# Kernel tuning notes

Hardware: AMD Instinct MI355X
Metric: run time of the kernel (lower is better)

Reference implementation:

```python
import jax, jax.numpy as jnp
import numpy as np

N, E, DIN, EDIM = 50000, 500000, 64, 32
H, C, L, NG = 4, 64, 2, 64
ND = 64  # node_dim (== C)
HC = H * C
EPS = 1e-5


def setup_inputs():
    key = jax.random.key(0)
    ks = iter(jax.random.split(key, 64))
    nxt = lambda: next(ks)
    inp = {
        "node_feature": jax.random.normal(nxt(), (N, DIN), jnp.float32),
        "edge_index": jax.random.randint(nxt(), (2, E), 0, N),
        "edge_feature": jax.random.normal(nxt(), (E, EDIM), jnp.float32),
        "batch": jnp.sort(jax.random.randint(nxt(), (N,), 0, NG)),
    }
    ins = [DIN, HC]
    for l in range(L):
        d = ins[l]
        s = 1.0 / np.sqrt(d)
        inp[f"Wl{l}"] = (jax.random.normal(nxt(), (d, HC)) * s).astype(jnp.float32)
        inp[f"bl{l}"] = jnp.zeros((HC,), jnp.float32)
        inp[f"Wr{l}"] = (jax.random.normal(nxt(), (d, HC)) * s).astype(jnp.float32)
        inp[f"br{l}"] = jnp.zeros((HC,), jnp.float32)
        inp[f"We{l}"] = (jax.random.normal(nxt(), (EDIM, HC)) * (1.0 / np.sqrt(EDIM))).astype(jnp.float32)
        inp[f"att{l}"] = (jax.random.normal(nxt(), (H, C)) * (1.0 / np.sqrt(C))).astype(jnp.float32)
        inp[f"bias{l}"] = jnp.zeros((HC,), jnp.float32)
    s2 = 1.0 / np.sqrt(HC)
    inp["node_W"] = (jax.random.normal(nxt(), (HC, ND)) * s2).astype(jnp.float32)
    inp["node_b"] = jnp.zeros((ND,), jnp.float32)
    inp["graph_W"] = (jax.random.normal(nxt(), (HC, ND)) * s2).astype(jnp.float32)
    inp["graph_b"] = jnp.zeros((ND,), jnp.float32)
    inp["nn_g"] = jnp.ones((ND,), jnp.float32)
    inp["nn_b"] = jnp.zeros((ND,), jnp.float32)
    inp["gn_g"] = jnp.ones((ND,), jnp.float32)
    inp["gn_b"] = jnp.zeros((ND,), jnp.float32)
    return inp


def _gatv2(x, src, dst, ea, Wl, bl, Wr, br, We, att, bias):
    # GATv2Conv (PyG defaults): self-loops with mean-filled edge_attr,
    # message m = leaky_relu(xl[src] + xr[dst] + lin_edge(ea)),
    # alpha = softmax_over_dst(<m, att>), out = sum_dst(xl[src] * alpha).
    n = x.shape[0]
    ones = jnp.ones((src.shape[0],), x.dtype)
    deg = jax.ops.segment_sum(ones, dst, num_segments=n)
    loop_attr = jax.ops.segment_sum(ea, dst, num_segments=n) / jnp.maximum(deg, 1.0)[:, None]
    loop = jnp.arange(n)
    srcf = jnp.concatenate([src, loop])
    dstf = jnp.concatenate([dst, loop])
    eaf = jnp.concatenate([ea, loop_attr], axis=0)
    xl = (x @ Wl + bl).reshape(n, H, C)
    xr = (x @ Wr + br).reshape(n, H, C)
    ee = (eaf @ We).reshape(-1, H, C)
    m = jax.nn.leaky_relu(xl[srcf] + xr[dstf] + ee, 0.2)  # [E', H, C]
    alpha = jnp.einsum('ehc,hc->eh', m, att)
    amax = jax.ops.segment_max(alpha, dstf, num_segments=n)
    a = jnp.exp(alpha - amax[dstf])
    denom = jax.ops.segment_sum(a, dstf, num_segments=n)
    a = a / denom[dstf]  # every node has a self-loop, denom > 0
    out = jax.ops.segment_sum(xl[srcf] * a[..., None], dstf, num_segments=n)
    return out.reshape(n, HC) + bias


def _layernorm(x, g, b):
    mu = x.mean(-1, keepdims=True)
    v = ((x - mu) ** 2).mean(-1, keepdims=True)
    return (x - mu) / jnp.sqrt(v + EPS) * g + b


def reference(node_feature, edge_index, edge_feature, batch, Wl0, bl0, Wr0, br0, We0, att0, bias0, Wl1, bl1, Wr1, br1, We1, att1, bias1, node_W, node_b, graph_W, graph_b, nn_g, nn_b, gn_g, gn_b):
    src, dst = edge_index[0], edge_index[1]
    x = _gatv2(node_feature, src, dst, edge_feature, Wl0, bl0, Wr0, br0, We0, att0, bias0)
    x = jax.nn.relu(x)
    x = _gatv2(x, src, dst, edge_feature, Wl1, bl1, Wr1, br1, We1, att1, bias1)
    local = _layernorm(x @ node_W + node_b, nn_g, nn_b)
    cnt = jax.ops.segment_sum(jnp.ones((x.shape[0],), x.dtype), batch, num_segments=NG)
    gmean = jax.ops.segment_sum(x, batch, num_segments=NG) / jnp.maximum(cnt, 1.0)[:, None]
    glob = _layernorm(gmean @ graph_W + graph_b, gn_g, gn_b)
    return local, glob
```

## Files before the change

### kernel.cpp

```cpp
#include <hip/hip_runtime.h>
#include <cstdint>
#include <cstddef>

#define NN   50000
#define NE   500000
#define DIN  64
#define EDIM 32
#define NH   4
#define NC   64
#define HC   256
#define NGG  64
#define ND   64
#define LN_EPS 1e-5f
#define EESLOTS (NE + NN)
#define XLR  512
#define SCAN_B   256
#define SCAN_NB  ((NN + SCAN_B - 1) / SCAN_B)

typedef __attribute__((ext_vector_type(8))) short bf16x8;
typedef __attribute__((ext_vector_type(4))) float f32x4;
typedef __attribute__((ext_vector_type(4))) unsigned short u16x4;
typedef _Float16 f16;
typedef __attribute__((ext_vector_type(4))) _Float16 f16x4;
typedef __attribute__((ext_vector_type(8))) _Float16 f16x8;

__device__ __forceinline__ unsigned short f2bf(float x) {
    unsigned u = __float_as_uint(x);
    unsigned r = (u + 0x7FFFu + ((u >> 16) & 1u)) >> 16;
    return (unsigned short)r;
}
__device__ __forceinline__ float bf2f(unsigned short h) {
    return __uint_as_float(((unsigned)h) << 16);
}

__global__ void count_deg(const int* __restrict__ dst, int* __restrict__ deg) {
    int e = blockIdx.x * blockDim.x + threadIdx.x;
    if (e < NE) atomicAdd(&deg[dst[e]], 1);
}

__global__ void scan_bsum(const int* __restrict__ deg, int* __restrict__ bsum) {
    __shared__ int s[SCAN_B];
    int t = threadIdx.x;
    int i = blockIdx.x * SCAN_B + t;
    s[t] = (i < NN) ? deg[i] : 0;
    __syncthreads();
    #pragma unroll
    for (int off = SCAN_B / 2; off > 0; off >>= 1) {
        if (t < off) s[t] += s[t + off];
        __syncthreads();
    }
    if (t == 0) bsum[blockIdx.x] = s[0];
}

__global__ void scan_boff(const int* __restrict__ bsum, int* __restrict__ boff) {
    __shared__ int s[SCAN_B];
    int t = threadIdx.x;
    int v = (t < SCAN_NB) ? bsum[t] : 0;
    s[t] = v;
    __syncthreads();
    #pragma unroll
    for (int off = 1; off < SCAN_B; off <<= 1) {
        int u = (t >= off) ? s[t - off] : 0;
        __syncthreads();
        s[t] += u;
        __syncthreads();
    }
    boff[t] = s[t] - v;
}

__global__ void scan_final(const int* __restrict__ deg, const int* __restrict__ boff,
                           int* __restrict__ row_ptr, int* __restrict__ cursor) {
    __shared__ int s[SCAN_B];
    int t = threadIdx.x;
    int i = blockIdx.x * SCAN_B + t;
    int v = (i < NN) ? deg[i] : 0;
    s[t] = v;
    __syncthreads();
    #pragma unroll
    for (int off = 1; off < SCAN_B; off <<= 1) {
        int u = (t >= off) ? s[t - off] : 0;
        __syncthreads();
        s[t] += u;
        __syncthreads();
    }
    int excl = boff[blockIdx.x] + s[t] - v;
    if (i < NN) {
        row_ptr[i] = excl;
        cursor[i] = excl;
    }
    if (i == 0) row_ptr[NN] = NE;
}

__global__ void fill_csr(const int* __restrict__ src, const int* __restrict__ dst,
                         int* __restrict__ cursor, int* __restrict__ csr_src,
                         int* __restrict__ csr_dst, int* __restrict__ csr_eid) {
    int e = blockIdx.x * blockDim.x + threadIdx.x;
    if (e < NE) {
        int d = dst[e];
        int pos = atomicAdd(&cursor[d], 1);
        csr_src[pos] = src[e];
        csr_dst[pos] = d;
        csr_eid[pos] = e;
    }
}

__global__ void perm_ef(const float* __restrict__ ef, const int* __restrict__ csr_eid,
                        const int* __restrict__ csr_src, const int* __restrict__ csr_dst,
                        f16* __restrict__ efp,
                        int* __restrict__ srcf, int* __restrict__ dstf) {
    int idx = blockIdx.x * blockDim.x + threadIdx.x;
    if (idx >= NE * 4) return;
    int j = idx >> 2, ch = idx & 3;
    int eid = csr_eid[j];
    const float* sp = ef + (size_t)eid * EDIM + ch * 8;
    float4 v0 = *(const float4*)sp;
    float4 v1 = *(const float4*)(sp + 4);
    f16x8 o;
    o[0] = (f16)v0.x; o[1] = (f16)v0.y; o[2] = (f16)v0.z; o[3] = (f16)v0.w;
    o[4] = (f16)v1.x; o[5] = (f16)v1.y; o[6] = (f16)v1.z; o[7] = (f16)v1.w;
    *(f16x8*)(efp + (size_t)j * EDIM + ch * 8) = o;
    if (ch == 0) { srcf[j] = csr_src[j]; dstf[j] = csr_dst[j]; }
}

__global__ void self_slots(const int* __restrict__ row_ptr,
                           f16* __restrict__ efp,
                           int* __restrict__ srcf, int* __restrict__ dstf) {
    int idx = blockIdx.x * blockDim.x + threadIdx.x;
    if (idx >= NN * EDIM) return;
    int n = idx >> 5, c = idx & 31;
    int s = row_ptr[n], e = row_ptr[n + 1];
    float acc = 0.f;
    for (int j = s; j < e; j++)
        acc += (float)efp[(size_t)j * EDIM + c];
    float m = acc / (float)max(e - s, 1);
    efp[(size_t)(NE + n) * EDIM + c] = (f16)m;
    if (c == 0) { srcf[NE + n] = n; dstf[NE + n] = n; }
}

__global__ void conv_wt(const float* __restrict__ W, unsigned short* __restrict__ hi,
                        unsigned short* __restrict__ lo, int K, int Nn) {
    int idx = blockIdx.x * blockDim.x + threadIdx.x;
    if (idx >= K * Nn) return;
    int k = idx / Nn, n = idx - k * Nn;
    float x = W[idx];
    unsigned short h = f2bf(x);
    unsigned short l = f2bf(x - bf2f(h));
    hi[(size_t)n * K + k] = h;
    lo[(size_t)n * K + k] = l;
}

__global__ void conv_wtf(const float* __restrict__ W, f16* __restrict__ o, int K, int Nn) {
    int idx = blockIdx.x * blockDim.x + threadIdx.x;
    if (idx >= K * Nn) return;
    int k = idx / Nn, n = idx - k * Nn;
    o[(size_t)n * K + k] = (f16)W[idx];
}

__global__ void conv_wet(const float* __restrict__ We, f16* __restrict__ wet) {
    int idx = blockIdx.x * blockDim.x + threadIdx.x;
    if (idx >= EDIM * HC) return;
    int k = idx / HC, c = idx - k * HC;
    int r = ((c & 15) << 4) | (c >> 4);
    wet[(size_t)r * EDIM + k] = (f16)We[idx];
}

__global__ void concat_bias(const float* __restrict__ a, const float* __restrict__ b,
                            float* __restrict__ o) {
    int i = threadIdx.x;
    o[i] = a[i];
    o[i + HC] = b[i];
}

#define LDT 40

__global__ __launch_bounds__(256, 2)
void gemm_wide(const float* __restrict__ A, const f16* __restrict__ Bt,
               const float* __restrict__ bias,
               f16* __restrict__ C, int M, int K) {
    __shared__ _Float16 Af[64][LDT];
    __shared__ _Float16 Bf[128][LDT];
    int tid = threadIdx.x;
    int lane = tid & 63, w = tid >> 6;
    int m = lane & 15, q = lane >> 4;
    int rowBase = blockIdx.y * 64, colBase = blockIdx.x * 128;
    f32x4 acc[8];
    #pragma unroll
    for (int ct = 0; ct < 8; ct++) acc[ct] = (f32x4){0.f, 0.f, 0.f, 0.f};

    for (int kk = 0; kk < K; kk += 32) {
        #pragma unroll
        for (int u = 0; u < 2; u++) {
            int f = tid + 256 * u;
            int r = f >> 3;
            int k4 = (f & 7) * 4;
            int row = rowBase + r;
            float4 v = make_float4(0.f, 0.f, 0.f, 0.f);
            if (row < M) v = *(const float4*)(A + (size_t)row * K + kk + k4);
            f16x4 h;
            h[0] = (f16)v.x; h[1] = (f16)v.y; h[2] = (f16)v.z; h[3] = (f16)v.w;
            *(f16x4*)&Af[r][k4] = h;
        }
        {
            int n = tid >> 1, hf = (tid & 1) * 16;
            size_t goff = (size_t)(colBase + n) * K + kk + hf;
            *(f16x8*)&Bf[n][hf]     = *(const f16x8*)(Bt + goff);
            *(f16x8*)&Bf[n][hf + 8] = *(const f16x8*)(Bt + goff + 8);
        }
        __syncthreads();
        f16x8 a = *(const f16x8*)&Af[w * 16 + m][q * 8];
        #pragma unroll
        for (int ct = 0; ct < 8; ct++) {
            f16x8 b = *(const f16x8*)&Bf[ct * 16 + m][q * 8];
            acc[ct] = __builtin_amdgcn_mfma_f32_16x16x32_f16(a, b, acc[ct], 0, 0, 0);
        }
        __syncthreads();
    }
    #pragma unroll
    for (int ct = 0; ct < 8; ct++) {
        int col = colBase + ct * 16 + m;
        float bb = bias[col];
        #pragma unroll
        for (int r = 0; r < 4; r++) {
            int row = rowBase + w * 16 + q * 4 + r;
            if (row < M) C[(size_t)row * XLR + col] = (f16)(acc[ct][r] + bb);
        }
    }
}

__global__ __launch_bounds__(256, 2)
void gemm_head(const float* __restrict__ A, const unsigned short* __restrict__ Bth,
               const unsigned short* __restrict__ Btl, const float* __restrict__ bias,
               float* __restrict__ C, int M, int K,
               const float* __restrict__ ln_g, const float* __restrict__ ln_b) {
    __shared__ unsigned short Ah[64][LDT], Al[64][LDT];
    __shared__ unsigned short Bh[64][LDT], Bl[64][LDT];
    int tid = threadIdx.x;
    int lane = tid & 63, w = tid >> 6;
    int m = lane & 15, q = lane >> 4;
    int rowBase = blockIdx.y * 64;
    f32x4 acc[4];
    #pragma unroll
    for (int ct = 0; ct < 4; ct++) acc[ct] = (f32x4){0.f, 0.f, 0.f, 0.f};

    for (int kk = 0; kk < K; kk += 32) {
        #pragma unroll
        for (int u = 0; u < 2; u++) {
            int f = tid + 256 * u;
            int r = f >> 3;
            int k4 = (f & 7) * 4;
            int row = rowBase + r;
            float4 v = make_float4(0.f, 0.f, 0.f, 0.f);
            if (row < M) v = *(const float4*)(A + (size_t)row * K + kk + k4);
            unsigned short h0 = f2bf(v.x), h1 = f2bf(v.y), h2 = f2bf(v.z), h3 = f2bf(v.w);
            unsigned short l0 = f2bf(v.x - bf2f(h0)), l1 = f2bf(v.y - bf2f(h1));
            unsigned short l2 = f2bf(v.z - bf2f(h2)), l3 = f2bf(v.w - bf2f(h3));
            *(u16x4*)&Ah[r][k4] = (u16x4){h0, h1, h2, h3};
            *(u16x4*)&Al[r][k4] = (u16x4){l0, l1, l2, l3};
        }
        {
            int n = tid >> 2;
            int ch = tid & 3;
            size_t goff = (size_t)n * K + kk + ch * 8;
            *(bf16x8*)&Bh[n][ch * 8] = *(const bf16x8*)(Bth + goff);
            *(bf16x8*)&Bl[n][ch * 8] = *(const bf16x8*)(Btl + goff);
        }
        __syncthreads();
        bf16x8 a_h = *(const bf16x8*)&Ah[w * 16 + m][q * 8];
        bf16x8 a_l = *(const bf16x8*)&Al[w * 16 + m][q * 8];
        #pragma unroll
        for (int ct = 0; ct < 4; ct++) {
            bf16x8 b_h = *(const bf16x8*)&Bh[ct * 16 + m][q * 8];
            bf16x8 b_l = *(const bf16x8*)&Bl[ct * 16 + m][q * 8];
            acc[ct] = __builtin_amdgcn_mfma_f32_16x16x32_bf16(a_h, b_h, acc[ct], 0, 0, 0);
            acc[ct] = __builtin_amdgcn_mfma_f32_16x16x32_bf16(a_l, b_h, acc[ct], 0, 0, 0);
            acc[ct] = __builtin_amdgcn_mfma_f32_16x16x32_bf16(a_h, b_l, acc[ct], 0, 0, 0);
        }
        __syncthreads();
    }
    #pragma unroll
    for (int r = 0; r < 4; r++) {
        float v[4];
        float sum = 0.f;
        #pragma unroll
        for (int ct = 0; ct < 4; ct++) {
            v[ct] = acc[ct][r] + bias[ct * 16 + m];
            sum += v[ct];
        }
        sum += __shfl_xor(sum, 1); sum += __shfl_xor(sum, 2);
        sum += __shfl_xor(sum, 4); sum += __shfl_xor(sum, 8);
        float mu = sum * (1.f / 64.f);
        float sq = 0.f;
        #pragma unroll
        for (int ct = 0; ct < 4; ct++) {
            float d = v[ct] - mu;
            sq += d * d;
        }
        sq += __shfl_xor(sq, 1); sq += __shfl_xor(sq, 2);
        sq += __shfl_xor(sq, 4); sq += __shfl_xor(sq, 8);
        float inv = rsqrtf(sq * (1.f / 64.f) + LN_EPS);
        int row = rowBase + w * 16 + q * 4 + r;
        if (row < M) {
            #pragma unroll
            for (int ct = 0; ct < 4; ct++) {
                int col = ct * 16 + m;
                C[(size_t)row * 64 + col] = (v[ct] - mu) * inv * ln_g[col] + ln_b[col];
            }
        }
    }
}

__global__ __launch_bounds__(256, 2)
void score_kernel(const f16* __restrict__ efp,
                  const int* __restrict__ srcf, const int* __restrict__ dstf,
                  const f16* __restrict__ xlr,
                  const f16* __restrict__ wet,
                  const float* __restrict__ att, float* __restrict__ alpha) {
    __shared__ _Float16 Af[64][LDT];
    __shared__ _Float16 Bf[256][LDT];
    __shared__ int s_src[64], s_dst[64];
    int tid = threadIdx.x;
    int lane = tid & 63, w = tid >> 6;
    int m = lane & 15, q = lane >> 4;

    #pragma unroll
    for (int u = 0; u < 4; u++) {
        *(f16x8*)&Bf[tid][u * 8] = *(const f16x8*)(wet + (size_t)tid * EDIM + u * 8);
    }
    float attv[16];
    #pragma unroll
    for (int u = 0; u < 4; u++) {
        float4 a4 = *(const float4*)(att + m * 16 + u * 4);
        attv[u * 4 + 0] = a4.x; attv[u * 4 + 1] = a4.y;
        attv[u * 4 + 2] = a4.z; attv[u * 4 + 3] = a4.w;
    }

    int groups = (EESLOTS + 63) >> 6;
    for (int g = blockIdx.x; g < groups; g += gridDim.x) {
        int base = g << 6;
        __syncthreads();
        {
            int r = tid >> 2, ch = tid & 3;
            int j = base + r;
            if (j >= EESLOTS) j = EESLOTS - 1;
            *(f16x8*)&Af[r][ch * 8] = *(const f16x8*)(efp + (size_t)j * EDIM + ch * 8);
            if (ch == 0) { s_src[r] = srcf[j]; s_dst[r] = dstf[j]; }
        }
        __syncthreads();

        f16x8 a = *(const f16x8*)&Af[w * 16 + m][q * 8];
        f32x4 acc[16];
        #pragma unroll
        for (int ct = 0; ct < 16; ct++) {
            f16x8 b = *(const f16x8*)&Bf[ct * 16 + m][q * 8];
            acc[ct] = __builtin_amdgcn_mfma_f32_16x16x32_f16(
                a, b, (f32x4){0.f, 0.f, 0.f, 0.f}, 0, 0, 0);
        }

        #pragma unroll
        for (int r = 0; r < 4; r++) {
            int sl = w * 16 + q * 4 + r;
            int slot = base + sl;
            int ss = s_src[sl], dd = s_dst[sl];
            const f16* xlp = xlr + (size_t)ss * XLR + m * 16;
            const f16* xrp = xlr + (size_t)dd * XLR + HC + m * 16;
            f16x8 xa0 = *(const f16x8*)(xlp);
            f16x8 xa1 = *(const f16x8*)(xlp + 8);
            f16x8 xb0 = *(const f16x8*)(xrp);
            f16x8 xb1 = *(const f16x8*)(xrp + 8);
            float s = 0.f;
            #pragma unroll
            for (int i = 0; i < 8; i++) {
                float z0 = (float)xa0[i] + (float)xb0[i] + acc[i][r];
                float lz0 = fmaxf(z0, 0.f) + 0.2f * fminf(z0, 0.f);
                s += lz0 * attv[i];
                float z1 = (float)xa1[i] + (float)xb1[i] + acc[8 + i][r];
                float lz1 = fmaxf(z1, 0.f) + 0.2f * fminf(z1, 0.f);
                s += lz1 * attv[8 + i];
            }
            s += __shfl_xor(s, 1);
            s += __shfl_xor(s, 2);
            if ((m & 3) == 0 && slot < EESLOTS) {
                alpha[(size_t)slot * 4 + (m >> 2)] = s;
            }
        }
    }
}

__global__ __launch_bounds__(256)
void gat_aggr(const f16* __restrict__ xlr, const float* __restrict__ alpha,
              const int* __restrict__ row_ptr, const int* __restrict__ csr_src,
              const float* __restrict__ bias, float* __restrict__ out, int do_relu) {
    int lane = threadIdx.x & 63;
    int wv = threadIdx.x >> 6;
    int n = blockIdx.x * 4 + wv;
    if (n >= NN) return;
    int h = lane >> 4;
    float4 bb = *(const float4*)(bias + 4 * lane);
    int s0 = row_ptr[n], e0 = row_ptr[n + 1];
    float aself = alpha[(size_t)(NE + n) * 4 + h];
    float denom = 1.f;
    f16x4 xs = *(const f16x4*)(xlr + (size_t)n * XLR + 4 * lane);
    float4 acc = make_float4((float)xs[0], (float)xs[1], (float)xs[2], (float)xs[3]);

    for (int j0 = s0; j0 < e0; j0 += 64) {
        int cnt = min(64, e0 - j0);
        int sidx = (j0 + lane < e0) ? csr_src[j0 + lane] : 0;
        int t = 0;
        for (; t + 3 < cnt; t += 4) {
            int sa = __shfl(sidx, t);
            int sb = __shfl(sidx, t + 1);
            int sc = __shfl(sidx, t + 2);
            int sd = __shfl(sidx, t + 3);
            float a0 = __expf(alpha[(size_t)(j0 + t) * 4 + h] - aself);
            float a1 = __expf(alpha[(size_t)(j0 + t + 1) * 4 + h] - aself);
            float a2 = __expf(alpha[(size_t)(j0 + t + 2) * 4 + h] - aself);
            float a3 = __expf(alpha[(size_t)(j0 + t + 3) * 4 + h] - aself);
            f16x4 x0 = *(const f16x4*)(xlr + (size_t)sa * XLR + 4 * lane);
            f16x4 x1 = *(const f16x4*)(xlr + (size_t)sb * XLR + 4 * lane);
            f16x4 x2 = *(const f16x4*)(xlr + (size_t)sc * XLR + 4 * lane);
            f16x4 x3 = *(const f16x4*)(xlr + (size_t)sd * XLR + 4 * lane);
            denom += a0 + a1 + a2 + a3;
            acc.x += a0 * (float)x0[0] + a1 * (float)x1[0] + a2 * (float)x2[0] + a3 * (float)x3[0];
            acc.y += a0 * (float)x0[1] + a1 * (float)x1[1] + a2 * (float)x2[1] + a3 * (float)x3[1];
            acc.z += a0 * (float)x0[2] + a1 * (float)x1[2] + a2 * (float)x2[2] + a3 * (float)x3[2];
            acc.w += a0 * (float)x0[3] + a1 * (float)x1[3] + a2 * (float)x2[3] + a3 * (float)x3[3];
        }
        for (; t < cnt; t++) {
            int sa = __shfl(sidx, t);
            float a0 = __expf(alpha[(size_t)(j0 + t) * 4 + h] - aself);
            f16x4 x0 = *(const f16x4*)(xlr + (size_t)sa * XLR + 4 * lane);
            denom += a0;
            acc.x += a0 * (float)x0[0]; acc.y += a0 * (float)x0[1];
            acc.z += a0 * (float)x0[2]; acc.w += a0 * (float)x0[3];
        }
    }

    float inv = 1.f / denom;
    float4 r = make_float4(acc.x * inv + bb.x, acc.y * inv + bb.y,
                           acc.z * inv + bb.z, acc.w * inv + bb.w);
    if (do_relu) {
        r.x = fmaxf(r.x, 0.f); r.y = fmaxf(r.y, 0.f);
        r.z = fmaxf(r.z, 0.f); r.w = fmaxf(r.w, 0.f);
    }
    *(float4*)(out + (size_t)n * HC + 4 * lane) = r;
}

__global__ void graph_sum(const float* __restrict__ x, const int* __restrict__ batch,
                          float* __restrict__ gsum, float* __restrict__ gcnt) {
    int c = threadIdx.x;
    int r0 = blockIdx.x * 64;
    int r1 = min(r0 + 64, NN);
    if (r0 >= NN) return;
    float acc = 0.f;
    int gcur = batch[r0];
    for (int n = r0; n < r1; n++) {
        int g = batch[n];
        if (g != gcur) {
            atomicAdd(&gsum[(size_t)gcur * HC + c], acc);
            acc = 0.f; gcur = g;
        }
        acc += x[(size_t)n * HC + c];
    }
    atomicAdd(&gsum[(size_t)gcur * HC + c], acc);
    if (c == 0) {
        int cnt = 0; gcur = batch[r0];
        for (int n = r0; n < r1; n++) {
            int g = batch[n];
            if (g != gcur) {
                atomicAdd(&gcnt[gcur], (float)cnt);
                cnt = 0; gcur = g;
            }
            cnt++;
        }
        atomicAdd(&gcnt[gcur], (float)cnt);
    }
}

__global__ void glob_kernel(const float* __restrict__ gsum, const float* __restrict__ gcnt,
                            const float* __restrict__ W, const float* __restrict__ bias,
                            const float* __restrict__ g, const float* __restrict__ b,
                            float* __restrict__ out) {
    int gi = blockIdx.x;
    int lane = threadIdx.x;
    float inv = 1.f / fmaxf(gcnt[gi], 1.f);
    float acc = 0.f;
    for (int k = 0; k < HC; k++)
        acc += (gsum[(size_t)gi * HC + k] * inv) * W[(size_t)k * ND + lane];
    acc += bias[lane];
    float s = acc;
    #pragma unroll
    for (int o = 32; o >= 1; o >>= 1) s += __shfl_xor(s, o);
    float mu = s * (1.f / 64.f);
    float dv = acc - mu;
    float q = dv * dv;
    #pragma unroll
    for (int o = 32; o >= 1; o >>= 1) q += __shfl_xor(q, o);
    float var = q * (1.f / 64.f);
    out[(size_t)gi * ND + lane] = dv * rsqrtf(var + LN_EPS) * g[lane] + b[lane];
}

extern "C" void kernel_launch(void* const* d_in, const int* in_sizes, int n_in,
                              void* d_out, int out_size, void* d_ws, size_t ws_size,
                              hipStream_t stream) {
    (void)in_sizes; (void)n_in; (void)out_size; (void)ws_size;
    const float* node_feature = (const float*)d_in[0];
    const int*   edge_index   = (const int*)d_in[1];
    const float* edge_feature = (const float*)d_in[2];
    const int*   batch        = (const int*)d_in[3];
    const float* Wl0   = (const float*)d_in[4];
    const float* bl0   = (const float*)d_in[5];
    const float* Wr0   = (const float*)d_in[6];
    const float* br0   = (const float*)d_in[7];
    const float* We0   = (const float*)d_in[8];
    const float* att0  = (const float*)d_in[9];
    const float* bias0 = (const float*)d_in[10];
    const float* Wl1   = (const float*)d_in[11];
    const float* bl1   = (const float*)d_in[12];
    const float* Wr1   = (const float*)d_in[13];
    const float* br1   = (const float*)d_in[14];
    const float* We1   = (const float*)d_in[15];
    const float* att1  = (const float*)d_in[16];
    const float* bias1 = (const float*)d_in[17];
    const float* node_W  = (const float*)d_in[18];
    const float* node_b  = (const float*)d_in[19];
    const float* graph_W = (const float*)d_in[20];
    const float* graph_b = (const float*)d_in[21];
    const float* nn_g = (const float*)d_in[22];
    const float* nn_b = (const float*)d_in[23];
    const float* gn_g = (const float*)d_in[24];
    const float* gn_b = (const float*)d_in[25];

    const int* src = edge_index;
    const int* dst = edge_index + NE;

    char* p = (char*)d_ws;
    auto carve = [&](size_t bytes) {
        char* r = p;
        p += (bytes + 255) & ~(size_t)255;
        return r;
    };
    int*   row_ptr   = (int*)carve((NN + 1) * sizeof(int));
    int*   cursor    = (int*)carve(NN * sizeof(int));
    int*   deg       = (int*)carve(NN * sizeof(int));
    int*   bsum      = (int*)carve(SCAN_B * sizeof(int));
    int*   boff      = (int*)carve(SCAN_B * sizeof(int));
    int*   csr_src   = (int*)carve((size_t)NE * sizeof(int));
    int*   csr_dst   = (int*)carve((size_t)NE * sizeof(int));
    int*   csr_eid   = (int*)carve((size_t)NE * sizeof(int));
    int*   srcf      = (int*)carve((size_t)EESLOTS * sizeof(int));
    int*   dstf      = (int*)carve((size_t)EESLOTS * sizeof(int));
    f16*   efp       = (f16*)carve((size_t)EESLOTS * EDIM * sizeof(f16));
    f16*   xlr       = (f16*)carve((size_t)NN * XLR * sizeof(f16));
    float* xb        = (float*)carve((size_t)NN * HC * sizeof(float));
    float* alpha     = (float*)carve((size_t)EESLOTS * NH * sizeof(float));
    float* gsum      = (float*)carve((size_t)(NGG * HC + NGG) * sizeof(float));
    float* gcnt      = gsum + (size_t)NGG * HC;
    f16* wlr0f = (f16*)carve((size_t)XLR * DIN * sizeof(f16));
    f16* wlr1f = (f16*)carve((size_t)XLR * HC * sizeof(f16));
    unsigned short* nwh   = (unsigned short*)carve((size_t)HC * ND * 2 * 2);
    unsigned short* nwl   = nwh + (size_t)HC * ND;
    f16* wet0 = (f16*)carve((size_t)EDIM * HC * sizeof(f16));
    f16* wet1 = (f16*)carve((size_t)EDIM * HC * sizeof(f16));
    float* b0cat = (float*)carve(XLR * sizeof(float));
    float* b1cat = (float*)carve(XLR * sizeof(float));

    hipMemsetAsync(deg, 0, NN * sizeof(int), stream);
    hipMemsetAsync(gsum, 0, (NGG * HC + NGG) * sizeof(float), stream);

    count_deg<<<(NE + 255) / 256, 256, 0, stream>>>(dst, deg);
    scan_bsum<<<SCAN_NB, SCAN_B, 0, stream>>>(deg, bsum);
    scan_boff<<<1, SCAN_B, 0, stream>>>(bsum, boff);
    scan_final<<<SCAN_NB, SCAN_B, 0, stream>>>(deg, boff, row_ptr, cursor);
    fill_csr<<<(NE + 255) / 256, 256, 0, stream>>>(src, dst, cursor, csr_src, csr_dst, csr_eid);
    perm_ef<<<(NE * 4 + 255) / 256, 256, 0, stream>>>(edge_feature, csr_eid, csr_src, csr_dst,
                                                      efp, srcf, dstf);
    self_slots<<<(NN * EDIM + 255) / 256, 256, 0, stream>>>(row_ptr, efp, srcf, dstf);
    conv_wtf<<<(DIN * HC + 255) / 256, 256, 0, stream>>>(Wl0, wlr0f, DIN, HC);
    conv_wtf<<<(DIN * HC + 255) / 256, 256, 0, stream>>>(Wr0, wlr0f + (size_t)HC * DIN, DIN, HC);
    conv_wtf<<<(HC * HC + 255) / 256, 256, 0, stream>>>(Wl1, wlr1f, HC, HC);
    conv_wtf<<<(HC * HC + 255) / 256, 256, 0, stream>>>(Wr1, wlr1f + (size_t)HC * HC, HC, HC);
    conv_wt<<<(HC * ND + 255) / 256, 256, 0, stream>>>(node_W, nwh, nwl, HC, ND);
    conv_wet<<<(EDIM * HC + 255) / 256, 256, 0, stream>>>(We0, wet0);
    conv_wet<<<(EDIM * HC + 255) / 256, 256, 0, stream>>>(We1, wet1);
    concat_bias<<<1, 256, 0, stream>>>(bl0, br0, b0cat);
    concat_bias<<<1, 256, 0, stream>>>(bl1, br1, b1cat);

    dim3 gw(4, (NN + 63) / 64);
    gemm_wide<<<gw, 256, 0, stream>>>(node_feature, wlr0f, b0cat, xlr, NN, DIN);
    score_kernel<<<2048, 256, 0, stream>>>(efp, srcf, dstf, xlr, wet0, att0, alpha);
    gat_aggr<<<(NN + 3) / 4, 256, 0, stream>>>(xlr, alpha, row_ptr, csr_src, bias0, xb, 1);
    gemm_wide<<<gw, 256, 0, stream>>>(xb, wlr1f, b1cat, xlr, NN, HC);
    score_kernel<<<2048, 256, 0, stream>>>(efp, srcf, dstf, xlr, wet1, att1, alpha);
    gat_aggr<<<(NN + 3) / 4, 256, 0, stream>>>(xlr, alpha, row_ptr, csr_src, bias1, xb, 0);

    float* out_local = (float*)d_out;
    float* out_glob  = out_local + (size_t)NN * ND;
    dim3 gh(1, (NN + 63) / 64);
    gemm_head<<<gh, 256, 0, stream>>>(xb, nwh, nwl, node_b, out_local, NN, HC, nn_g, nn_b);
    graph_sum<<<(NN + 63) / 64, 256, 0, stream>>>(xb, batch, gsum, gcnt);
    glob_kernel<<<NGG, 64, 0, stream>>>(gsum, gcnt, graph_W, graph_b, gn_g, gn_b, out_glob);
}
```

Before: 605.3 us.

## Split xl/xr into separate buffers and use packed fp16 math in score kernel

The interleaved [N,512] xl|xr buffer becomes two separate [N,256] buffers. Gathers of xl in the score and aggregation kernels now touch a denser array with better cache-line locality. The score kernel also does the add, leaky-relu and attention dot product in packed fp16 using fdot2 instead of scalar fp32. This cuts ALU work but lowers the precision of the attention logits.

```diff
diff --git a/kernel.cpp b/kernel.cpp
--- a/kernel.cpp
+++ b/kernel.cpp
@@ -13,7 +13,6 @@
 #define ND   64
 #define LN_EPS 1e-5f
 #define EESLOTS (NE + NN)
-#define XLR  512
 #define SCAN_B   256
 #define SCAN_NB  ((NN + SCAN_B - 1) / SCAN_B)
 
@@ -21,6 +20,7 @@
 typedef __attribute__((ext_vector_type(4))) float f32x4;
 typedef __attribute__((ext_vector_type(4))) unsigned short u16x4;
 typedef _Float16 f16;
+typedef __attribute__((ext_vector_type(2))) _Float16 f16x2;
 typedef __attribute__((ext_vector_type(4))) _Float16 f16x4;
 typedef __attribute__((ext_vector_type(8))) _Float16 f16x8;
 
@@ -176,7 +176,7 @@
 __global__ __launch_bounds__(256, 2)
 void gemm_wide(const float* __restrict__ A, const f16* __restrict__ Bt,
                const float* __restrict__ bias,
-               f16* __restrict__ C, int M, int K) {
+               f16* __restrict__ xlb, f16* __restrict__ xrb, int M, int K) {
     __shared__ _Float16 Af[64][LDT];
     __shared__ _Float16 Bf[128][LDT];
     int tid = threadIdx.x;
@@ -215,14 +215,17 @@
         }
         __syncthreads();
     }
+    f16* ob = (colBase < HC) ? xlb : xrb;
+    int obase = (colBase < HC) ? colBase : colBase - HC;
     #pragma unroll
     for (int ct = 0; ct < 8; ct++) {
         int col = colBase + ct * 16 + m;
+        int ocol = obase + ct * 16 + m;
         float bb = bias[col];
         #pragma unroll
         for (int r = 0; r < 4; r++) {
             int row = rowBase + w * 16 + q * 4 + r;
-            if (row < M) C[(size_t)row * XLR + col] = (f16)(acc[ct][r] + bb);
+            if (row < M) ob[(size_t)row * HC + ocol] = (f16)(acc[ct][r] + bb);
         }
     }
 }
@@ -312,7 +315,7 @@
 __global__ __launch_bounds__(256, 2)
 void score_kernel(const f16* __restrict__ efp,
                   const int* __restrict__ srcf, const int* __restrict__ dstf,
-                  const f16* __restrict__ xlr,
+                  const f16* __restrict__ xlb, const f16* __restrict__ xrb,
                   const f16* __restrict__ wet,
                   const float* __restrict__ att, float* __restrict__ alpha) {
     __shared__ _Float16 Af[64][LDT];
@@ -326,13 +329,14 @@
     for (int u = 0; u < 4; u++) {
         *(f16x8*)&Bf[tid][u * 8] = *(const f16x8*)(wet + (size_t)tid * EDIM + u * 8);
     }
-    float attv[16];
-    #pragma unroll
-    for (int u = 0; u < 4; u++) {
-        float4 a4 = *(const float4*)(att + m * 16 + u * 4);
-        attv[u * 4 + 0] = a4.x; attv[u * 4 + 1] = a4.y;
-        attv[u * 4 + 2] = a4.z; attv[u * 4 + 3] = a4.w;
-    }
+    f16x8 attp0, attp1;
+    #pragma unroll
+    for (int i = 0; i < 8; i++) {
+        attp0[i] = (f16)att[m * 16 + i];
+        attp1[i] = (f16)att[m * 16 + 8 + i];
+    }
+
+    const f16x8 zero8 = {(f16)0, (f16)0, (f16)0, (f16)0, (f16)0, (f16)0, (f16)0, (f16)0};
 
     int groups = (EESLOTS + 63) >> 6;
     for (int g = blockIdx.x; g < groups; g += gridDim.x) {
@@ -361,22 +365,45 @@
             int sl = w * 16 + q * 4 + r;
             int slot = base + sl;
             int ss = s_src[sl], dd = s_dst[sl];
-            const f16* xlp = xlr + (size_t)ss * XLR + m * 16;
-            const f16* xrp = xlr + (size_t)dd * XLR + HC + m * 16;
+            const f16* xlp = xlb + (size_t)ss * HC + m * 16;
+            const f16* xrp = xrb + (size_t)dd * HC + m * 16;
             f16x8 xa0 = *(const f16x8*)(xlp);
             f16x8 xa1 = *(const f16x8*)(xlp + 8);
             f16x8 xb0 = *(const f16x8*)(xrp);
             f16x8 xb1 = *(const f16x8*)(xrp + 8);
-            float s = 0.f;
+            f16x8 z0 = xa0 + xb0;
+            f16x8 z1 = xa1 + xb1;
+            f16x8 e0, e1;
             #pragma unroll
             for (int i = 0; i < 8; i++) {
-                float z0 = (float)xa0[i] + (float)xb0[i] + acc[i][r];
-                float lz0 = fmaxf(z0, 0.f) + 0.2f * fminf(z0, 0.f);
-                s += lz0 * attv[i];
-                float z1 = (float)xa1[i] + (float)xb1[i] + acc[8 + i][r];
-                float lz1 = fmaxf(z1, 0.f) + 0.2f * fminf(z1, 0.f);
-                s += lz1 * attv[8 + i];
+                e0[i] = (f16)acc[i][r];
+                e1[i] = (f16)acc[8 + i][r];
             }
+            z0 += e0;
+            z1 += e1;
+            f16x8 lz0 = __builtin_elementwise_min(z0, zero8) * (f16)0.2f
+                      + __builtin_elementwise_max(z0, zero8);
+            f16x8 lz1 = __builtin_elementwise_min(z1, zero8) * (f16)0.2f
+                      + __builtin_elementwise_max(z1, zero8);
+            float s0 = 0.f, s1 = 0.f;
+#if __has_builtin(__builtin_amdgcn_fdot2)
+            #pragma unroll
+            for (int i = 0; i < 4; i++) {
+                f16x2 a2 = {lz0[2 * i], lz0[2 * i + 1]};
+                f16x2 b2 = {attp0[2 * i], attp0[2 * i + 1]};
+                s0 = __builtin_amdgcn_fdot2(a2, b2, s0, false);
+                f16x2 c2 = {lz1[2 * i], lz1[2 * i + 1]};
+                f16x2 d2 = {attp1[2 * i], attp1[2 * i + 1]};
+                s1 = __builtin_amdgcn_fdot2(c2, d2, s1, false);
+            }
+#else
+            #pragma unroll
+            for (int i = 0; i < 8; i++) {
+                s0 += (float)lz0[i] * (float)attp0[i];
+                s1 += (float)lz1[i] * (float)attp1[i];
+            }
+#endif
+            float s = s0 + s1;
             s += __shfl_xor(s, 1);
             s += __shfl_xor(s, 2);
             if ((m & 3) == 0 && slot < EESLOTS) {
@@ -387,7 +414,7 @@
 }
 
 __global__ __launch_bounds__(256)
-void gat_aggr(const f16* __restrict__ xlr, const float* __restrict__ alpha,
+void gat_aggr(const f16* __restrict__ xlb, const float* __restrict__ alpha,
               const int* __restrict__ row_ptr, const int* __restrict__ csr_src,
               const float* __restrict__ bias, float* __restrict__ out, int do_relu) {
     int lane = threadIdx.x & 63;
@@ -399,7 +426,7 @@
     int s0 = row_ptr[n], e0 = row_ptr[n + 1];
     float aself = alpha[(size_t)(NE + n) * 4 + h];
     float denom = 1.f;
-    f16x4 xs = *(const f16x4*)(xlr + (size_t)n * XLR + 4 * lane);
+    f16x4 xs = *(const f16x4*)(xlb + (size_t)n * HC + 4 * lane);
     float4 acc = make_float4((float)xs[0], (float)xs[1], (float)xs[2], (float)xs[3]);
 
     for (int j0 = s0; j0 < e0; j0 += 64) {
@@ -415,10 +442,10 @@
             float a1 = __expf(alpha[(size_t)(j0 + t + 1) * 4 + h] - aself);
             float a2 = __expf(alpha[(size_t)(j0 + t + 2) * 4 + h] - aself);
             float a3 = __expf(alpha[(size_t)(j0 + t + 3) * 4 + h] - aself);
-            f16x4 x0 = *(const f16x4*)(xlr + (size_t)sa * XLR + 4 * lane);
-            f16x4 x1 = *(const f16x4*)(xlr + (size_t)sb * XLR + 4 * lane);
-            f16x4 x2 = *(const f16x4*)(xlr + (size_t)sc * XLR + 4 * lane);
-            f16x4 x3 = *(const f16x4*)(xlr + (size_t)sd * XLR + 4 * lane);
+            f16x4 x0 = *(const f16x4*)(xlb + (size_t)sa * HC + 4 * lane);
+            f16x4 x1 = *(const f16x4*)(xlb + (size_t)sb * HC + 4 * lane);
+            f16x4 x2 = *(const f16x4*)(xlb + (size_t)sc * HC + 4 * lane);
+            f16x4 x3 = *(const f16x4*)(xlb + (size_t)sd * HC + 4 * lane);
             denom += a0 + a1 + a2 + a3;
             acc.x += a0 * (float)x0[0] + a1 * (float)x1[0] + a2 * (float)x2[0] + a3 * (float)x3[0];
             acc.y += a0 * (float)x0[1] + a1 * (float)x1[1] + a2 * (float)x2[1] + a3 * (float)x3[1];
@@ -428,7 +455,7 @@
         for (; t < cnt; t++) {
             int sa = __shfl(sidx, t);
             float a0 = __expf(alpha[(size_t)(j0 + t) * 4 + h] - aself);
-            f16x4 x0 = *(const f16x4*)(xlr + (size_t)sa * XLR + 4 * lane);
+            f16x4 x0 = *(const f16x4*)(xlb + (size_t)sa * HC + 4 * lane);
             denom += a0;
             acc.x += a0 * (float)x0[0]; acc.y += a0 * (float)x0[1];
             acc.z += a0 * (float)x0[2]; acc.w += a0 * (float)x0[3];
@@ -550,19 +577,20 @@
     int*   srcf      = (int*)carve((size_t)EESLOTS * sizeof(int));
     int*   dstf      = (int*)carve((size_t)EESLOTS * sizeof(int));
     f16*   efp       = (f16*)carve((size_t)EESLOTS * EDIM * sizeof(f16));
-    f16*   xlr       = (f16*)carve((size_t)NN * XLR * sizeof(f16));
+    f16*   xlb       = (f16*)carve((size_t)NN * HC * sizeof(f16));
+    f16*   xrb       = (f16*)carve((size_t)NN * HC * sizeof(f16));
     float* xb        = (float*)carve((size_t)NN * HC * sizeof(float));
     float* alpha     = (float*)carve((size_t)EESLOTS * NH * sizeof(float));
     float* gsum      = (float*)carve((size_t)(NGG * HC + NGG) * sizeof(float));
     float* gcnt      = gsum + (size_t)NGG * HC;
-    f16* wlr0f = (f16*)carve((size_t)XLR * DIN * sizeof(f16));
-    f16* wlr1f = (f16*)carve((size_t)XLR * HC * sizeof(f16));
+    f16* wlr0f = (f16*)carve((size_t)(2 * HC) * DIN * sizeof(f16));
+    f16* wlr1f = (f16*)carve((size_t)(2 * HC) * HC * sizeof(f16));
     unsigned short* nwh   = (unsigned short*)carve((size_t)HC * ND * 2 * 2);
     unsigned short* nwl   = nwh + (size_t)HC * ND;
     f16* wet0 = (f16*)carve((size_t)EDIM * HC * sizeof(f16));
     f16* wet1 = (f16*)carve((size_t)EDIM * HC * sizeof(f16));
-    float* b0cat = (float*)carve(XLR * sizeof(float));
-    float* b1cat = (float*)carve(XLR * sizeof(float));
+    float* b0cat = (float*)carve(2 * HC * sizeof(float));
+    float* b1cat = (float*)carve(2 * HC * sizeof(float));
 
     hipMemsetAsync(deg, 0, NN * sizeof(int), stream);
     hipMemsetAsync(gsum, 0, (NGG * HC + NGG) * sizeof(float), stream);
@@ -586,12 +614,12 @@
     concat_bias<<<1, 256, 0, stream>>>(bl1, br1, b1cat);
 
     dim3 gw(4, (NN + 63) / 64);
-    gemm_wide<<<gw, 256, 0, stream>>>(node_feature, wlr0f, b0cat, xlr, NN, DIN);
-    score_kernel<<<2048, 256, 0, stream>>>(efp, srcf, dstf, xlr, wet0, att0, alpha);
-    gat_aggr<<<(NN + 3) / 4, 256, 0, stream>>>(xlr, alpha, row_ptr, csr_src, bias0, xb, 1);
-    gemm_wide<<<gw, 256, 0, stream>>>(xb, wlr1f, b1cat, xlr, NN, HC);
-    score_kernel<<<2048, 256, 0, stream>>>(efp, srcf, dstf, xlr, wet1, att1, alpha);
-    gat_aggr<<<(NN + 3) / 4, 256, 0, stream>>>(xlr, alpha, row_ptr, csr_src, bias1, xb, 0);
+    gemm_wide<<<gw, 256, 0, stream>>>(node_feature, wlr0f, b0cat, xlb, xrb, NN, DIN);
+    score_kernel<<<2048, 256, 0, stream>>>(efp, srcf, dstf, xlb, xrb, wet0, att0, alpha);
+    gat_aggr<<<(NN + 3) / 4, 256, 0, stream>>>(xlb, alpha, row_ptr, csr_src, bias0, xb, 1);
+    gemm_wide<<<gw, 256, 0, stream>>>(xb, wlr1f, b1cat, xlb, xrb, NN, HC);
+    score_kernel<<<2048, 256, 0, stream>>>(efp, srcf, dstf, xlb, xrb, wet1, att1, alpha);
+    gat_aggr<<<(NN + 3) / 4, 256, 0, stream>>>(xlb, alpha, row_ptr, csr_src, bias1, xb, 0);
 
     float* out_local = (float*)d_out;
     float* out_glob  = out_local + (size_t)NN * ND;
```

After: 604.2 us. No clear change (-0.2%).
